# Performance work log

Measured on AMD Instinct MI355X. Metric: run time of the kernel, lower is better.

Reference implementation:

```python
import jax, jax.numpy as jnp
import numpy as np

B, S, D, H = 16, 512, 1024, 16
DK = D // H  # 64
HEAD_SCALE = DK ** -0.5


def setup_inputs() -> dict:
    key = jax.random.key(0)
    ks = jax.random.split(key, 8)
    std = D ** -0.5
    return {
        "Q": jax.random.normal(ks[0], (B, S, D), jnp.float32),
        "prev": jax.random.normal(ks[1], (B, H, S, S), jnp.float32) * 0.1,
        "Wq": jax.random.normal(ks[2], (D, D), jnp.float32) * std,
        "bq": jnp.zeros((D,), jnp.float32),
        "Wk": jax.random.normal(ks[3], (D, D), jnp.float32) * std,
        "bk": jnp.zeros((D,), jnp.float32),
        "Wv": jax.random.normal(ks[4], (D, D), jnp.float32) * std,
        "bv": jnp.zeros((D,), jnp.float32),
        "Wg": jax.random.normal(ks[5], (D, H * S), jnp.float32) * std,
        "bg": jnp.zeros((H * S,), jnp.float32),
        "Wo": jax.random.normal(ks[6], (D, D), jnp.float32) * std,
        "bo": jnp.zeros((D,), jnp.float32),
        "scale": jnp.asarray(HEAD_SCALE, jnp.float32),
    }


def reference(Q, prev, Wq, bq, Wk, bk, Wv, bv, Wg, bg, Wo, bo, scale):
    bs = Q.shape[0]
    # projections -> [bs, n_heads, seq, head_dim]
    q = (Q @ Wq + bq).reshape(bs, S, H, DK).transpose(0, 2, 1, 3)
    k = (Q @ Wk + bk).reshape(bs, S, H, DK).transpose(0, 2, 1, 3)
    v = (Q @ Wv + bv).reshape(bs, S, H, DK).transpose(0, 2, 1, 3)
    # gating: G_V(Q).view(bs, S, H, S).transpose(1,2) -> [bs, H, S, S]
    g = (Q @ Wg + bg).reshape(bs, S, H, S).transpose(0, 2, 1, 3)
    # residual-attention scores
    scores = jnp.einsum("bhqd,bhkd->bhqk", q, k) * scale + prev
    attn = g * jax.nn.softmax(scores, axis=-1)  # gated attention weights
    out = jnp.einsum("bhqk,bhkd->bhqd", attn, v)
    out = out.transpose(0, 2, 1, 3).reshape(bs, S, H * DK)
    out = out @ Wo + bo
    return out, attn, scores
```

## Files before the change

kernel.cpp:

```cpp
#include <hip/hip_runtime.h>

#define SEQ    512
#define NH     16
#define HDIM   64
#define DMODEL 1024
#define MROWS  8192
#define OUT_ELEMS   8388608ll
#define ATTN_ELEMS  67108864ll

typedef __attribute__((ext_vector_type(8))) short short8;
typedef __attribute__((ext_vector_type(4))) float f32x4;

__device__ __forceinline__ ushort f2bf(float x) {
    unsigned u = __float_as_uint(x);
    u += 0x7FFFu + ((u >> 16) & 1u);
    return (ushort)(u >> 16);
}
__device__ __forceinline__ float bf2f(ushort h) {
    return __uint_as_float(((unsigned)h) << 16);
}
__device__ __forceinline__ unsigned pack2(ushort a, ushort b) {
    return (unsigned)a | ((unsigned)b << 16);
}

__global__ __launch_bounds__(256)
void split_kernel(const float* __restrict__ X, ushort* __restrict__ hi,
                  ushort* __restrict__ lo)
{
    size_t base = ((size_t)blockIdx.x * 256 + threadIdx.x) * 8;
    float4 x0 = *(const float4*)&X[base];
    float4 x1 = *(const float4*)&X[base + 4];
    float xs[8] = {x0.x, x0.y, x0.z, x0.w, x1.x, x1.y, x1.z, x1.w};
    ushort h[8], l[8];
#pragma unroll
    for (int i = 0; i < 8; ++i) {
        h[i] = f2bf(xs[i]);
        l[i] = f2bf(xs[i] - bf2f(h[i]));
    }
    uint4 uh, ul;
    uh.x = pack2(h[0], h[1]); uh.y = pack2(h[2], h[3]);
    uh.z = pack2(h[4], h[5]); uh.w = pack2(h[6], h[7]);
    ul.x = pack2(l[0], l[1]); ul.y = pack2(l[2], l[3]);
    ul.z = pack2(l[4], l[5]); ul.w = pack2(l[6], l[7]);
    *(uint4*)&hi[base] = uh;
    *(uint4*)&lo[base] = ul;
}

__global__ __launch_bounds__(256)
void splitT_kernel(const float* __restrict__ W, ushort* __restrict__ th,
                   ushort* __restrict__ tl, int N, int K)
{
    const int t   = threadIdx.x;
    const int col = blockIdx.x * 64 + (t & 63);
    const int kb  = blockIdx.y * 64 + (t >> 6) * 16;
    ushort h[16], l[16];
#pragma unroll
    for (int i = 0; i < 16; ++i) {
        float x = W[(size_t)(kb + i) * N + col];
        h[i] = f2bf(x);
        l[i] = f2bf(x - bf2f(h[i]));
    }
    size_t o = (size_t)col * K + kb;
    uint4 u;
    u.x = pack2(h[0], h[1]);  u.y = pack2(h[2], h[3]);
    u.z = pack2(h[4], h[5]);  u.w = pack2(h[6], h[7]);
    *(uint4*)&th[o] = u;
    u.x = pack2(h[8], h[9]);  u.y = pack2(h[10], h[11]);
    u.z = pack2(h[12], h[13]); u.w = pack2(h[14], h[15]);
    *(uint4*)&th[o + 8] = u;
    u.x = pack2(l[0], l[1]);  u.y = pack2(l[2], l[3]);
    u.z = pack2(l[4], l[5]);  u.w = pack2(l[6], l[7]);
    *(uint4*)&tl[o] = u;
    u.x = pack2(l[8], l[9]);  u.y = pack2(l[10], l[11]);
    u.z = pack2(l[12], l[13]); u.w = pack2(l[14], l[15]);
    *(uint4*)&tl[o + 8] = u;
}

__global__ __launch_bounds__(256)
void gemm_mfma(const ushort* __restrict__ Ahi, const ushort* __restrict__ Alo,
               const ushort* __restrict__ Bhi, const ushort* __restrict__ Blo,
               const float* __restrict__ bias, float* __restrict__ Cdst,
               int K, int Hn, int cl)
{
    __shared__ ushort sA[2][128][40];
    __shared__ ushort sB[2][128][40];

    const int t    = threadIdx.x;
    const int i0   = blockIdx.y * 128;
    const int j0   = blockIdx.x * 128;
    const int lane = t & 63, wid = t >> 6;
    const int wr = wid >> 1, wc = wid & 1;
    const int ln = lane & 15, ko = (lane >> 4) * 8;

    f32x4 acc[4][4];
#pragma unroll
    for (int m = 0; m < 4; ++m)
#pragma unroll
        for (int n = 0; n < 4; ++n) acc[m][n] = (f32x4){0.f, 0.f, 0.f, 0.f};

    const int row_s = t >> 2;
    const int kq_s  = (t & 3) * 8;

    for (int k0 = 0; k0 < K; k0 += 32) {
#pragma unroll
        for (int l = 0; l < 2; ++l) {
            int row = row_s + l * 64;
            size_t ga = (size_t)(i0 + row) * K + k0 + kq_s;
            *(uint4*)&sA[0][row][kq_s] = *(const uint4*)&Ahi[ga];
            *(uint4*)&sA[1][row][kq_s] = *(const uint4*)&Alo[ga];
            size_t gb = (size_t)(j0 + row) * K + k0 + kq_s;
            *(uint4*)&sB[0][row][kq_s] = *(const uint4*)&Bhi[gb];
            *(uint4*)&sB[1][row][kq_s] = *(const uint4*)&Blo[gb];
        }
        __syncthreads();

        short8 ah[4], al[4];
#pragma unroll
        for (int m = 0; m < 4; ++m) {
            ah[m] = *(const short8*)&sA[0][wr * 64 + m * 16 + ln][ko];
            al[m] = *(const short8*)&sA[1][wr * 64 + m * 16 + ln][ko];
        }
#pragma unroll
        for (int n = 0; n < 4; ++n) {
            short8 bh = *(const short8*)&sB[0][wc * 64 + n * 16 + ln][ko];
            short8 bl = *(const short8*)&sB[1][wc * 64 + n * 16 + ln][ko];
#pragma unroll
            for (int m = 0; m < 4; ++m) {
                acc[m][n] = __builtin_amdgcn_mfma_f32_16x16x32_bf16(ah[m], bh, acc[m][n], 0, 0, 0);
                acc[m][n] = __builtin_amdgcn_mfma_f32_16x16x32_bf16(al[m], bh, acc[m][n], 0, 0, 0);
                acc[m][n] = __builtin_amdgcn_mfma_f32_16x16x32_bf16(ah[m], bl, acc[m][n], 0, 0, 0);
            }
        }
        __syncthreads();
    }

    const int chunk = 1 << cl;
#pragma unroll
    for (int n = 0; n < 4; ++n) {
        int j = j0 + wc * 64 + n * 16 + ln;
        int h = j >> cl, c = j & (chunk - 1);
        float bv = bias[j];
#pragma unroll
        for (int m = 0; m < 4; ++m) {
#pragma unroll
            for (int r = 0; r < 4; ++r) {
                int i  = i0 + wr * 64 + m * 16 + (lane >> 4) * 4 + r;
                int bb = i >> 9, s = i & 511;
                Cdst[((size_t)(bb * Hn + h) * SEQ + s) * chunk + c] = acc[m][n][r] + bv;
            }
        }
    }
}

__global__ __launch_bounds__(256)
void scores_kernel(const float* __restrict__ q_ws, const float* __restrict__ k_ws,
                   const float* __restrict__ prev, const float* __restrict__ scale_p,
                   float* __restrict__ scores)
{
    const int bid   = blockIdx.x;
    const int batch = bid >> 6;
    const int tile  = bid & 63;
    const int i0    = (tile >> 3) * 64;
    const int j0    = (tile & 7) * 64;
    const float* q = q_ws + (size_t)batch * SEQ * HDIM;
    const float* k = k_ws + (size_t)batch * SEQ * HDIM;
    const float scale = *scale_p;

    __shared__ float sA[16][68];
    __shared__ float sB[16][68];
    const int t = threadIdx.x;
    const int ty = t >> 4, tx = t & 15;
    float acc[4][4] = {};

    for (int k0 = 0; k0 < HDIM; k0 += 16) {
        int row = t >> 2, c4 = (t & 3) * 4;
        float4 va = *(const float4*)&q[(size_t)(i0 + row) * HDIM + k0 + c4];
        sA[c4 + 0][row] = va.x; sA[c4 + 1][row] = va.y;
        sA[c4 + 2][row] = va.z; sA[c4 + 3][row] = va.w;
        float4 vb = *(const float4*)&k[(size_t)(j0 + row) * HDIM + k0 + c4];
        sB[c4 + 0][row] = vb.x; sB[c4 + 1][row] = vb.y;
        sB[c4 + 2][row] = vb.z; sB[c4 + 3][row] = vb.w;
        __syncthreads();
#pragma unroll
        for (int kk = 0; kk < 16; ++kk) {
            float4 a = *(const float4*)&sA[kk][ty * 4];
            float4 b = *(const float4*)&sB[kk][tx * 4];
            float ra[4] = {a.x, a.y, a.z, a.w};
            float rb[4] = {b.x, b.y, b.z, b.w};
#pragma unroll
            for (int x = 0; x < 4; ++x)
#pragma unroll
                for (int y = 0; y < 4; ++y) acc[x][y] += ra[x] * rb[y];
        }
        __syncthreads();
    }

#pragma unroll
    for (int x = 0; x < 4; ++x) {
        int i = i0 + ty * 4 + x;
        size_t base = ((size_t)batch * SEQ + i) * SEQ + j0 + tx * 4;
        float4 pv = *(const float4*)&prev[base];
        float4 r;
        r.x = acc[x][0] * scale + pv.x;
        r.y = acc[x][1] * scale + pv.y;
        r.z = acc[x][2] * scale + pv.z;
        r.w = acc[x][3] * scale + pv.w;
        *(float4*)&scores[base] = r;
    }
}

__global__ __launch_bounds__(256)
void softmax_gate(const float* __restrict__ scores, float* __restrict__ attn)
{
    const int row = blockIdx.x * 4 + (threadIdx.x >> 6);
    const int l   = threadIdx.x & 63;
    const size_t base = (size_t)row * SEQ;

    float4 x0 = *(const float4*)&scores[base + l * 4];
    float4 x1 = *(const float4*)&scores[base + 256 + l * 4];
    float xs[8] = {x0.x, x0.y, x0.z, x0.w, x1.x, x1.y, x1.z, x1.w};

    float m = xs[0];
#pragma unroll
    for (int i = 1; i < 8; ++i) m = fmaxf(m, xs[i]);
#pragma unroll
    for (int o = 1; o < 64; o <<= 1) m = fmaxf(m, __shfl_xor(m, o));

    float es[8];
    float sum = 0.f;
#pragma unroll
    for (int i = 0; i < 8; ++i) { es[i] = __expf(xs[i] - m); sum += es[i]; }
#pragma unroll
    for (int o = 1; o < 64; o <<= 1) sum += __shfl_xor(sum, o);
    const float inv = 1.0f / sum;

    float4 g0 = *(const float4*)&attn[base + l * 4];
    float4 g1 = *(const float4*)&attn[base + 256 + l * 4];
    float4 r0, r1;
    r0.x = g0.x * es[0] * inv; r0.y = g0.y * es[1] * inv;
    r0.z = g0.z * es[2] * inv; r0.w = g0.w * es[3] * inv;
    r1.x = g1.x * es[4] * inv; r1.y = g1.y * es[5] * inv;
    r1.z = g1.z * es[6] * inv; r1.w = g1.w * es[7] * inv;
    *(float4*)&attn[base + l * 4]       = r0;
    *(float4*)&attn[base + 256 + l * 4] = r1;
}

__global__ __launch_bounds__(256)
void pv_kernel(const float* __restrict__ attn, const float* __restrict__ v_ws,
               float* __restrict__ o_ws)
{
    const int bid   = blockIdx.x;
    const int batch = bid >> 3;
    const int i0    = (bid & 7) * 64;
    const float* A = attn + (size_t)batch * SEQ * SEQ;
    const float* V = v_ws + (size_t)batch * SEQ * HDIM;
    const int b = batch >> 4, h = batch & 15;

    __shared__ float sA[16][68];
    __shared__ float sB[16][64];
    const int t = threadIdx.x;
    const int ty = t >> 4, tx = t & 15;
    float acc[4][4] = {};

    for (int k0 = 0; k0 < SEQ; k0 += 16) {
        int row = t >> 2, c4 = (t & 3) * 4;
        float4 va = *(const float4*)&A[(size_t)(i0 + row) * SEQ + k0 + c4];
        sA[c4 + 0][row] = va.x; sA[c4 + 1][row] = va.y;
        sA[c4 + 2][row] = va.z; sA[c4 + 3][row] = va.w;
        int r = t >> 4, c44 = (t & 15) * 4;
        *(float4*)&sB[r][c44] = *(const float4*)&V[(size_t)(k0 + r) * HDIM + c44];
        __syncthreads();
#pragma unroll
        for (int kk = 0; kk < 16; ++kk) {
            float4 a = *(const float4*)&sA[kk][ty * 4];
            float4 bv = *(const float4*)&sB[kk][tx * 4];
            float ra[4] = {a.x, a.y, a.z, a.w};
            float rb[4] = {bv.x, bv.y, bv.z, bv.w};
#pragma unroll
            for (int x = 0; x < 4; ++x)
#pragma unroll
                for (int y = 0; y < 4; ++y) acc[x][y] += ra[x] * rb[y];
        }
        __syncthreads();
    }

#pragma unroll
    for (int x = 0; x < 4; ++x) {
        int i = i0 + ty * 4 + x;
        size_t dst = ((size_t)(b * SEQ + i) * NH + h) * HDIM + tx * 4;
        float4 r = {acc[x][0], acc[x][1], acc[x][2], acc[x][3]};
        *(float4*)&o_ws[dst] = r;
    }
}

extern "C" void kernel_launch(void* const* d_in, const int* in_sizes, int n_in,
                              void* d_out, int out_size, void* d_ws, size_t ws_size,
                              hipStream_t stream)
{
    const float* Q     = (const float*)d_in[0];
    const float* prev  = (const float*)d_in[1];
    const float* Wq    = (const float*)d_in[2];
    const float* bq    = (const float*)d_in[3];
    const float* Wk    = (const float*)d_in[4];
    const float* bk    = (const float*)d_in[5];
    const float* Wv    = (const float*)d_in[6];
    const float* bv    = (const float*)d_in[7];
    const float* Wg    = (const float*)d_in[8];
    const float* bg    = (const float*)d_in[9];
    const float* Wo    = (const float*)d_in[10];
    const float* bo    = (const float*)d_in[11];
    const float* scale = (const float*)d_in[12];

    float* out    = (float*)d_out;
    float* attn   = out + OUT_ELEMS;
    float* scores = attn + ATTN_ELEMS;

    float* q_ws = (float*)d_ws;
    float* k_ws = q_ws + OUT_ELEMS;
    float* v_ws = k_ws + OUT_ELEMS;
    float* o_ws = q_ws;

    const size_t U1M = 1048576;
    ushort* sc16 = (ushort*)scores;
    ushort* WtQh = sc16 + 0 * U1M;
    ushort* WtQl = sc16 + 1 * U1M;
    ushort* WtKh = sc16 + 2 * U1M;
    ushort* WtKl = sc16 + 3 * U1M;
    ushort* WtVh = sc16 + 4 * U1M;
    ushort* WtVl = sc16 + 5 * U1M;
    ushort* WtGh = sc16 + 6 * U1M;
    ushort* WtGl = sc16 + 14 * U1M;
    ushort* Qh   = sc16 + 22 * U1M;
    ushort* Ql   = sc16 + 30 * U1M;

    ushort* Oh   = (ushort*)k_ws;
    ushort* Ol   = Oh + OUT_ELEMS;
    ushort* WtOh = (ushort*)v_ws;
    ushort* WtOl = WtOh + U1M;

    dim3 blk(256);

    splitT_kernel<<<dim3(16, 16), blk, 0, stream>>>(Wq, WtQh, WtQl, DMODEL, DMODEL);
    splitT_kernel<<<dim3(16, 16), blk, 0, stream>>>(Wk, WtKh, WtKl, DMODEL, DMODEL);
    splitT_kernel<<<dim3(16, 16), blk, 0, stream>>>(Wv, WtVh, WtVl, DMODEL, DMODEL);
    splitT_kernel<<<dim3(128, 16), blk, 0, stream>>>(Wg, WtGh, WtGl, 8192, DMODEL);
    split_kernel<<<4096, blk, 0, stream>>>(Q, Qh, Ql);

    gemm_mfma<<<dim3(8, 64), blk, 0, stream>>>(Qh, Ql, WtQh, WtQl, bq, q_ws, DMODEL, NH, 6);
    gemm_mfma<<<dim3(8, 64), blk, 0, stream>>>(Qh, Ql, WtKh, WtKl, bk, k_ws, DMODEL, NH, 6);
    gemm_mfma<<<dim3(8, 64), blk, 0, stream>>>(Qh, Ql, WtVh, WtVl, bv, v_ws, DMODEL, NH, 6);
    gemm_mfma<<<dim3(64, 64), blk, 0, stream>>>(Qh, Ql, WtGh, WtGl, bg, attn, DMODEL, NH, 9);

    scores_kernel<<<256 * 64, blk, 0, stream>>>(q_ws, k_ws, prev, scale, scores);
    softmax_gate<<<(16 * NH * SEQ) / 4, blk, 0, stream>>>(scores, attn);
    pv_kernel<<<256 * 8, blk, 0, stream>>>(attn, v_ws, o_ws);

    split_kernel<<<4096, blk, 0, stream>>>(o_ws, Oh, Ol);
    splitT_kernel<<<dim3(16, 16), blk, 0, stream>>>(Wo, WtOh, WtOl, DMODEL, DMODEL);
    gemm_mfma<<<dim3(8, 64), blk, 0, stream>>>(Oh, Ol, WtOh, WtOl, bo, out, DMODEL, 1, 10);
}
```

Measured before the change: 1.722 ms.

## Move scores and PV batched GEMMs to split-bf16 MFMA kernels

Replaces the scalar FP32 shared-memory GEMMs for QK^T scores and attn·V with MFMA kernels. Inputs are split on the fly into bf16 hi/lo parts and three bf16 MFMAs are used to approximate FP32 accuracy. Tiles are enlarged to 128x128 for scores and 128x64 for PV. A shared split helper is factored out. The aim is to cut FP32 ALU cost. In exchange, the epilogue stores become scalar and strided rather than float4, and the result carries slight precision loss from dropping the lo×lo term.

```diff
diff --git a/kernel.cpp b/kernel.cpp
--- a/kernel.cpp
+++ b/kernel.cpp
@@ -23,27 +23,32 @@
     return (unsigned)a | ((unsigned)b << 16);
 }
 
+__device__ __forceinline__ void split8_to(const float* __restrict__ src,
+                                          ushort* dh, ushort* dl) {
+    float4 x0 = *(const float4*)src;
+    float4 x1 = *(const float4*)(src + 4);
+    float xs[8] = {x0.x, x0.y, x0.z, x0.w, x1.x, x1.y, x1.z, x1.w};
+    ushort hh[8], ll[8];
+#pragma unroll
+    for (int i = 0; i < 8; ++i) {
+        hh[i] = f2bf(xs[i]);
+        ll[i] = f2bf(xs[i] - bf2f(hh[i]));
+    }
+    uint4 uh, ul;
+    uh.x = pack2(hh[0], hh[1]); uh.y = pack2(hh[2], hh[3]);
+    uh.z = pack2(hh[4], hh[5]); uh.w = pack2(hh[6], hh[7]);
+    ul.x = pack2(ll[0], ll[1]); ul.y = pack2(ll[2], ll[3]);
+    ul.z = pack2(ll[4], ll[5]); ul.w = pack2(ll[6], ll[7]);
+    *(uint4*)dh = uh;
+    *(uint4*)dl = ul;
+}
+
 __global__ __launch_bounds__(256)
 void split_kernel(const float* __restrict__ X, ushort* __restrict__ hi,
                   ushort* __restrict__ lo)
 {
     size_t base = ((size_t)blockIdx.x * 256 + threadIdx.x) * 8;
-    float4 x0 = *(const float4*)&X[base];
-    float4 x1 = *(const float4*)&X[base + 4];
-    float xs[8] = {x0.x, x0.y, x0.z, x0.w, x1.x, x1.y, x1.z, x1.w};
-    ushort h[8], l[8];
-#pragma unroll
-    for (int i = 0; i < 8; ++i) {
-        h[i] = f2bf(xs[i]);
-        l[i] = f2bf(xs[i] - bf2f(h[i]));
-    }
-    uint4 uh, ul;
-    uh.x = pack2(h[0], h[1]); uh.y = pack2(h[2], h[3]);
-    uh.z = pack2(h[4], h[5]); uh.w = pack2(h[6], h[7]);
-    ul.x = pack2(l[0], l[1]); ul.y = pack2(l[2], l[3]);
-    ul.z = pack2(l[4], l[5]); ul.w = pack2(l[6], l[7]);
-    *(uint4*)&hi[base] = uh;
-    *(uint4*)&lo[base] = ul;
+    split8_to(&X[base], &hi[base], &lo[base]);
 }
 
 __global__ __launch_bounds__(256)
@@ -153,59 +158,79 @@
 }
 
 __global__ __launch_bounds__(256)
-void scores_kernel(const float* __restrict__ q_ws, const float* __restrict__ k_ws,
-                   const float* __restrict__ prev, const float* __restrict__ scale_p,
-                   float* __restrict__ scores)
+void scores_mfma(const float* __restrict__ q_ws, const float* __restrict__ k_ws,
+                 const float* __restrict__ prev, const float* __restrict__ scale_p,
+                 float* __restrict__ scores)
 {
     const int bid   = blockIdx.x;
-    const int batch = bid >> 6;
-    const int tile  = bid & 63;
-    const int i0    = (tile >> 3) * 64;
-    const int j0    = (tile & 7) * 64;
+    const int batch = bid >> 4;
+    const int tile  = bid & 15;
+    const int i0    = (tile >> 2) * 128;
+    const int j0    = (tile & 3) * 128;
     const float* q = q_ws + (size_t)batch * SEQ * HDIM;
     const float* k = k_ws + (size_t)batch * SEQ * HDIM;
     const float scale = *scale_p;
 
-    __shared__ float sA[16][68];
-    __shared__ float sB[16][68];
-    const int t = threadIdx.x;
-    const int ty = t >> 4, tx = t & 15;
-    float acc[4][4] = {};
-
-    for (int k0 = 0; k0 < HDIM; k0 += 16) {
-        int row = t >> 2, c4 = (t & 3) * 4;
-        float4 va = *(const float4*)&q[(size_t)(i0 + row) * HDIM + k0 + c4];
-        sA[c4 + 0][row] = va.x; sA[c4 + 1][row] = va.y;
-        sA[c4 + 2][row] = va.z; sA[c4 + 3][row] = va.w;
-        float4 vb = *(const float4*)&k[(size_t)(j0 + row) * HDIM + k0 + c4];
-        sB[c4 + 0][row] = vb.x; sB[c4 + 1][row] = vb.y;
-        sB[c4 + 2][row] = vb.z; sB[c4 + 3][row] = vb.w;
-        __syncthreads();
-#pragma unroll
-        for (int kk = 0; kk < 16; ++kk) {
-            float4 a = *(const float4*)&sA[kk][ty * 4];
-            float4 b = *(const float4*)&sB[kk][tx * 4];
-            float ra[4] = {a.x, a.y, a.z, a.w};
-            float rb[4] = {b.x, b.y, b.z, b.w};
-#pragma unroll
-            for (int x = 0; x < 4; ++x)
-#pragma unroll
-                for (int y = 0; y < 4; ++y) acc[x][y] += ra[x] * rb[y];
-        }
-        __syncthreads();
-    }
-
-#pragma unroll
-    for (int x = 0; x < 4; ++x) {
-        int i = i0 + ty * 4 + x;
-        size_t base = ((size_t)batch * SEQ + i) * SEQ + j0 + tx * 4;
-        float4 pv = *(const float4*)&prev[base];
-        float4 r;
-        r.x = acc[x][0] * scale + pv.x;
-        r.y = acc[x][1] * scale + pv.y;
-        r.z = acc[x][2] * scale + pv.z;
-        r.w = acc[x][3] * scale + pv.w;
-        *(float4*)&scores[base] = r;
+    __shared__ ushort sA[2][128][40];
+    __shared__ ushort sB[2][128][40];
+
+    const int t    = threadIdx.x;
+    const int lane = t & 63, wid = t >> 6;
+    const int wr = wid >> 1, wc = wid & 1;
+    const int ln = lane & 15, ko = (lane >> 4) * 8;
+
+    f32x4 acc[4][4];
+#pragma unroll
+    for (int m = 0; m < 4; ++m)
+#pragma unroll
+        for (int n = 0; n < 4; ++n) acc[m][n] = (f32x4){0.f, 0.f, 0.f, 0.f};
+
+    const int row_s = t >> 2;
+    const int kq_s  = (t & 3) * 8;
+
+    for (int k0 = 0; k0 < HDIM; k0 += 32) {
+#pragma unroll
+        for (int l = 0; l < 2; ++l) {
+            int row = row_s + l * 64;
+            split8_to(&q[(size_t)(i0 + row) * HDIM + k0 + kq_s],
+                      &sA[0][row][kq_s], &sA[1][row][kq_s]);
+            split8_to(&k[(size_t)(j0 + row) * HDIM + k0 + kq_s],
+                      &sB[0][row][kq_s], &sB[1][row][kq_s]);
+        }
+        __syncthreads();
+
+        short8 ah[4], al[4];
+#pragma unroll
+        for (int m = 0; m < 4; ++m) {
+            ah[m] = *(const short8*)&sA[0][wr * 64 + m * 16 + ln][ko];
+            al[m] = *(const short8*)&sA[1][wr * 64 + m * 16 + ln][ko];
+        }
+#pragma unroll
+        for (int n = 0; n < 4; ++n) {
+            short8 bh = *(const short8*)&sB[0][wc * 64 + n * 16 + ln][ko];
+            short8 bl = *(const short8*)&sB[1][wc * 64 + n * 16 + ln][ko];
+#pragma unroll
+            for (int m = 0; m < 4; ++m) {
+                acc[m][n] = __builtin_amdgcn_mfma_f32_16x16x32_bf16(ah[m], bh, acc[m][n], 0, 0, 0);
+                acc[m][n] = __builtin_amdgcn_mfma_f32_16x16x32_bf16(al[m], bh, acc[m][n], 0, 0, 0);
+                acc[m][n] = __builtin_amdgcn_mfma_f32_16x16x32_bf16(ah[m], bl, acc[m][n], 0, 0, 0);
+            }
+        }
+        __syncthreads();
+    }
+
+#pragma unroll
+    for (int n = 0; n < 4; ++n) {
+        int j = j0 + wc * 64 + n * 16 + ln;
+#pragma unroll
+        for (int m = 0; m < 4; ++m) {
+#pragma unroll
+            for (int r = 0; r < 4; ++r) {
+                int i = i0 + wr * 64 + m * 16 + (lane >> 4) * 4 + r;
+                size_t idx = ((size_t)batch * SEQ + i) * SEQ + j;
+                scores[idx] = acc[m][n][r] * scale + prev[idx];
+            }
+        }
     }
 }
 
@@ -246,50 +271,86 @@
 }
 
 __global__ __launch_bounds__(256)
-void pv_kernel(const float* __restrict__ attn, const float* __restrict__ v_ws,
-               float* __restrict__ o_ws)
+void pv_mfma(const float* __restrict__ attn, const float* __restrict__ v_ws,
+             float* __restrict__ o_ws)
 {
     const int bid   = blockIdx.x;
-    const int batch = bid >> 3;
-    const int i0    = (bid & 7) * 64;
+    const int batch = bid >> 2;
+    const int i0    = (bid & 3) * 128;
+    const int b = batch >> 4, h = batch & 15;
     const float* A = attn + (size_t)batch * SEQ * SEQ;
     const float* V = v_ws + (size_t)batch * SEQ * HDIM;
-    const int b = batch >> 4, h = batch & 15;
-
-    __shared__ float sA[16][68];
-    __shared__ float sB[16][64];
-    const int t = threadIdx.x;
-    const int ty = t >> 4, tx = t & 15;
-    float acc[4][4] = {};
-
-    for (int k0 = 0; k0 < SEQ; k0 += 16) {
-        int row = t >> 2, c4 = (t & 3) * 4;
-        float4 va = *(const float4*)&A[(size_t)(i0 + row) * SEQ + k0 + c4];
-        sA[c4 + 0][row] = va.x; sA[c4 + 1][row] = va.y;
-        sA[c4 + 2][row] = va.z; sA[c4 + 3][row] = va.w;
-        int r = t >> 4, c44 = (t & 15) * 4;
-        *(float4*)&sB[r][c44] = *(const float4*)&V[(size_t)(k0 + r) * HDIM + c44];
-        __syncthreads();
-#pragma unroll
-        for (int kk = 0; kk < 16; ++kk) {
-            float4 a = *(const float4*)&sA[kk][ty * 4];
-            float4 bv = *(const float4*)&sB[kk][tx * 4];
-            float ra[4] = {a.x, a.y, a.z, a.w};
-            float rb[4] = {bv.x, bv.y, bv.z, bv.w};
-#pragma unroll
-            for (int x = 0; x < 4; ++x)
-#pragma unroll
-                for (int y = 0; y < 4; ++y) acc[x][y] += ra[x] * rb[y];
-        }
-        __syncthreads();
-    }
-
-#pragma unroll
-    for (int x = 0; x < 4; ++x) {
-        int i = i0 + ty * 4 + x;
-        size_t dst = ((size_t)(b * SEQ + i) * NH + h) * HDIM + tx * 4;
-        float4 r = {acc[x][0], acc[x][1], acc[x][2], acc[x][3]};
-        *(float4*)&o_ws[dst] = r;
+
+    __shared__ ushort sA[2][128][40];
+    __shared__ ushort sB[2][64][40];
+
+    const int t    = threadIdx.x;
+    const int lane = t & 63, wid = t >> 6;
+    const int ln = lane & 15, ko = (lane >> 4) * 8;
+
+    f32x4 acc[2][4];
+#pragma unroll
+    for (int m = 0; m < 2; ++m)
+#pragma unroll
+        for (int n = 0; n < 4; ++n) acc[m][n] = (f32x4){0.f, 0.f, 0.f, 0.f};
+
+    const int row_s = t >> 2;
+    const int kq_s  = (t & 3) * 8;
+    const int vk = t >> 3;
+    const int vd = (t & 7) * 8;
+
+    for (int k0 = 0; k0 < SEQ; k0 += 32) {
+#pragma unroll
+        for (int l = 0; l < 2; ++l) {
+            int row = row_s + l * 64;
+            split8_to(&A[(size_t)(i0 + row) * SEQ + k0 + kq_s],
+                      &sA[0][row][kq_s], &sA[1][row][kq_s]);
+        }
+        {
+            const float* vp = &V[(size_t)(k0 + vk) * HDIM + vd];
+            float4 x0 = *(const float4*)vp;
+            float4 x1 = *(const float4*)(vp + 4);
+            float xs[8] = {x0.x, x0.y, x0.z, x0.w, x1.x, x1.y, x1.z, x1.w};
+#pragma unroll
+            for (int j = 0; j < 8; ++j) {
+                ushort hh = f2bf(xs[j]);
+                sB[0][vd + j][vk] = hh;
+                sB[1][vd + j][vk] = f2bf(xs[j] - bf2f(hh));
+            }
+        }
+        __syncthreads();
+
+        short8 ah[2], al[2];
+#pragma unroll
+        for (int m = 0; m < 2; ++m) {
+            ah[m] = *(const short8*)&sA[0][wid * 32 + m * 16 + ln][ko];
+            al[m] = *(const short8*)&sA[1][wid * 32 + m * 16 + ln][ko];
+        }
+#pragma unroll
+        for (int n = 0; n < 4; ++n) {
+            short8 bh = *(const short8*)&sB[0][n * 16 + ln][ko];
+            short8 bl = *(const short8*)&sB[1][n * 16 + ln][ko];
+#pragma unroll
+            for (int m = 0; m < 2; ++m) {
+                acc[m][n] = __builtin_amdgcn_mfma_f32_16x16x32_bf16(ah[m], bh, acc[m][n], 0, 0, 0);
+                acc[m][n] = __builtin_amdgcn_mfma_f32_16x16x32_bf16(al[m], bh, acc[m][n], 0, 0, 0);
+                acc[m][n] = __builtin_amdgcn_mfma_f32_16x16x32_bf16(ah[m], bl, acc[m][n], 0, 0, 0);
+            }
+        }
+        __syncthreads();
+    }
+
+#pragma unroll
+    for (int n = 0; n < 4; ++n) {
+        int d = n * 16 + ln;
+#pragma unroll
+        for (int m = 0; m < 2; ++m) {
+#pragma unroll
+            for (int r = 0; r < 4; ++r) {
+                int s = i0 + wid * 32 + m * 16 + (lane >> 4) * 4 + r;
+                o_ws[((size_t)(b * SEQ + s) * NH + h) * HDIM + d] = acc[m][n][r];
+            }
+        }
     }
 }
 
@@ -351,9 +412,9 @@
     gemm_mfma<<<dim3(8, 64), blk, 0, stream>>>(Qh, Ql, WtVh, WtVl, bv, v_ws, DMODEL, NH, 6);
     gemm_mfma<<<dim3(64, 64), blk, 0, stream>>>(Qh, Ql, WtGh, WtGl, bg, attn, DMODEL, NH, 9);
 
-    scores_kernel<<<256 * 64, blk, 0, stream>>>(q_ws, k_ws, prev, scale, scores);
+    scores_mfma<<<4096, blk, 0, stream>>>(q_ws, k_ws, prev, scale, scores);
     softmax_gate<<<(16 * NH * SEQ) / 4, blk, 0, stream>>>(scores, attn);
-    pv_kernel<<<256 * 8, blk, 0, stream>>>(attn, v_ws, o_ws);
+    pv_mfma<<<1024, blk, 0, stream>>>(attn, v_ws, o_ws);
 
     split_kernel<<<4096, blk, 0, stream>>>(o_ws, Oh, Ol);
     splitT_kernel<<<dim3(16, 16), blk, 0, stream>>>(Wo, WtOh, WtOl, DMODEL, DMODEL);
```

Result: no change. 1.726 ms (+0.2%).
